# Kernel tuning notes

Measured on AMD Instinct MI355X. Metric: run time of the kernel, lower is better.

Reference implementation:

```python
import jax, jax.numpy as jnp
import numpy as np

N, E, D, R = 50000, 800000, 128, 200


def setup_inputs() -> dict:
    key = jax.random.key(0)
    ks = jax.random.split(key, 8)
    h = jax.random.normal(ks[0], (N, D), jnp.float32)
    emb_rel = jax.random.normal(ks[1], (R, D), jnp.float32)
    loop_weight = jax.random.normal(ks[2], (D, D), jnp.float32) * 0.05
    attn_fc_w = jax.random.normal(ks[3], (D, 3 * D), jnp.float32) * 0.05  # Linear(3D,D) weight [D,3D]
    attn_fc2_w = jax.random.normal(ks[4], (1, D), jnp.float32) * 0.05     # Linear(D,1) weight [1,D]
    src = jax.random.randint(ks[5], (E,), 0, N)
    dst = jax.random.randint(ks[6], (E,), 0, N)
    etype = jax.random.randint(ks[7], (E,), 0, R)
    return {"h": h, "emb_rel": emb_rel, "loop_weight": loop_weight,
            "attn_fc_w": attn_fc_w, "attn_fc2_w": attn_fc2_w,
            "src": src, "dst": dst, "etype": etype}


def reference(h, emb_rel, loop_weight, attn_fc_w, attn_fc2_w, src, dst, etype):
    num_nodes = h.shape[0]
    # attn_fc(concat([h_src, h_dst, rel])) == h_src@Ws.T + h_dst@Wd.T + rel@Wr.T
    # (avoids materializing the [E, 3D] concat)
    Ws, Wd, Wr = jnp.split(attn_fc_w, 3, axis=1)  # each [D, D]
    hs = h[src]  # [E, D] gathered source features
    a = hs @ Ws.T + h[dst] @ Wd.T + emb_rel[etype] @ Wr.T  # [E, D]
    e = jax.nn.leaky_relu((a @ attn_fc2_w.T)[:, 0], 0.01)  # [E] edge logits
    # segment softmax over destination node (stable)
    m = jax.ops.segment_max(e, dst, num_segments=num_nodes)
    w = jnp.exp(e - m[dst])
    denom = jax.ops.segment_sum(w, dst, num_segments=num_nodes)
    alpha = w / denom[dst]  # [E]
    # weighted scatter-sum of source features into destination nodes
    agg = jax.ops.segment_sum(alpha[:, None] * hs, dst, num_segments=num_nodes)
    # DGL update_all leaves zero-in-degree nodes' feature unchanged
    deg = jax.ops.segment_sum(jnp.ones_like(e), dst, num_segments=num_nodes)
    agg = jnp.where(deg[:, None] > 0, agg, h)
    # self-loop message
    return agg + h @ loop_weight
```

## Files before the change

### kernel.cpp

```cpp
#include <hip/hip_runtime.h>

#define D 128
#define TD 384
#define TN 64
#define U  8

__global__ void k_prep(const float* __restrict__ A, const float* __restrict__ v,
                       float* __restrict__ p) {
  __shared__ float vs[D];
  int t = threadIdx.x;
  if (t < D) vs[t] = v[t];
  __syncthreads();
  float acc = 0.f;
#pragma unroll 8
  for (int i = 0; i < D; ++i) acc += vs[i] * A[i * TD + t];
  p[t] = acc;
}

__global__ __launch_bounds__(256) void k_sl(const float* __restrict__ h,
                                            const float* __restrict__ lw,
                                            float* __restrict__ sl, int N) {
  __shared__ float W[D * D];
  int t = threadIdx.x;
  for (int i = t; i < D * D / 4; i += 256)
    ((float4*)W)[i] = ((const float4*)lw)[i];
  __syncthreads();
  int qc = t & 31;
  int slot = t >> 5;
  int ntiles = (N + TN - 1) / TN;
  for (int tile = blockIdx.x; tile < ntiles; tile += gridDim.x) {
    int base = tile * TN + slot * U;
    float4 acc[U];
#pragma unroll
    for (int u = 0; u < U; ++u) acc[u] = make_float4(0.f, 0.f, 0.f, 0.f);
    if ((tile + 1) * TN <= N) {
      for (int k4 = 0; k4 < D / 4; ++k4) {
        int k = k4 * 4;
        float4 w0 = ((const float4*)(W + (size_t)(k + 0) * D))[qc];
        float4 w1 = ((const float4*)(W + (size_t)(k + 1) * D))[qc];
        float4 w2 = ((const float4*)(W + (size_t)(k + 2) * D))[qc];
        float4 w3 = ((const float4*)(W + (size_t)(k + 3) * D))[qc];
#pragma unroll
        for (int u = 0; u < U; ++u) {
          float4 hv = *(const float4*)(h + (size_t)(base + u) * D + k);
          acc[u].x = fmaf(hv.x, w0.x, fmaf(hv.y, w1.x, fmaf(hv.z, w2.x, fmaf(hv.w, w3.x, acc[u].x))));
          acc[u].y = fmaf(hv.x, w0.y, fmaf(hv.y, w1.y, fmaf(hv.z, w2.y, fmaf(hv.w, w3.y, acc[u].y))));
          acc[u].z = fmaf(hv.x, w0.z, fmaf(hv.y, w1.z, fmaf(hv.z, w2.z, fmaf(hv.w, w3.z, acc[u].z))));
          acc[u].w = fmaf(hv.x, w0.w, fmaf(hv.y, w1.w, fmaf(hv.z, w2.w, fmaf(hv.w, w3.w, acc[u].w))));
        }
      }
#pragma unroll
      for (int u = 0; u < U; ++u)
        ((float4*)(sl + (size_t)(base + u) * D))[qc] = acc[u];
    } else {
      for (int k4 = 0; k4 < D / 4; ++k4) {
        int k = k4 * 4;
        float4 w0 = ((const float4*)(W + (size_t)(k + 0) * D))[qc];
        float4 w1 = ((const float4*)(W + (size_t)(k + 1) * D))[qc];
        float4 w2 = ((const float4*)(W + (size_t)(k + 2) * D))[qc];
        float4 w3 = ((const float4*)(W + (size_t)(k + 3) * D))[qc];
#pragma unroll
        for (int u = 0; u < U; ++u) {
          if (base + u < N) {
            float4 hv = *(const float4*)(h + (size_t)(base + u) * D + k);
            acc[u].x = fmaf(hv.x, w0.x, fmaf(hv.y, w1.x, fmaf(hv.z, w2.x, fmaf(hv.w, w3.x, acc[u].x))));
            acc[u].y = fmaf(hv.x, w0.y, fmaf(hv.y, w1.y, fmaf(hv.z, w2.y, fmaf(hv.w, w3.y, acc[u].y))));
            acc[u].z = fmaf(hv.x, w0.z, fmaf(hv.y, w1.z, fmaf(hv.z, w2.z, fmaf(hv.w, w3.z, acc[u].z))));
            acc[u].w = fmaf(hv.x, w0.w, fmaf(hv.y, w1.w, fmaf(hv.z, w2.w, fmaf(hv.w, w3.w, acc[u].w))));
          }
        }
      }
#pragma unroll
      for (int u = 0; u < U; ++u)
        if (base + u < N)
          ((float4*)(sl + (size_t)(base + u) * D))[qc] = acc[u];
    }
  }
}

__global__ void k_scores_hist(const float* __restrict__ h, const float* __restrict__ emb,
                              const float* __restrict__ p, const int* __restrict__ dst,
                              float* __restrict__ ss, float* __restrict__ sd,
                              float* __restrict__ sr, int* __restrict__ cnt,
                              int N, int R, int E, int nbScore) {
  int t = threadIdx.x;
  if ((int)blockIdx.x < nbScore) {
    __shared__ float pl[TD];
    pl[t] = p[t];
    if (t < TD - 256) pl[256 + t] = p[256 + t];
    __syncthreads();
    int w = blockIdx.x * 4 + (t >> 6);
    int l = t & 63;
    if (w < N) {
      float x0 = h[(size_t)w * D + l];
      float x1 = h[(size_t)w * D + 64 + l];
      float a = x0 * pl[l] + x1 * pl[64 + l];
      float b = x0 * pl[128 + l] + x1 * pl[192 + l];
#pragma unroll
      for (int o = 32; o; o >>= 1) { a += __shfl_xor(a, o); b += __shfl_xor(b, o); }
      if (l == 0) { ss[w] = a; sd[w] = b; }
    } else if (w < N + R) {
      int r = w - N;
      float x0 = emb[(size_t)r * D + l];
      float x1 = emb[(size_t)r * D + 64 + l];
      float c = x0 * pl[256 + l] + x1 * pl[320 + l];
#pragma unroll
      for (int o = 32; o; o >>= 1) c += __shfl_xor(c, o);
      if (l == 0) sr[r] = c;
    }
  } else {
    int i = (blockIdx.x - nbScore) * 256 + t;
    int stride = (gridDim.x - nbScore) * 256;
    for (; i < E; i += stride) atomicAdd(&cnt[dst[i]], 1);
  }
}

__global__ void k_scan1(int* __restrict__ cnt, int* __restrict__ bsum, int N) {
  __shared__ int wsum[16];
  int t = threadIdx.x, lane = t & 63, wid = t >> 6;
  int i = blockIdx.x * 1024 + t;
  int v = (i < N) ? cnt[i] : 0;
  int x = v;
#pragma unroll
  for (int o = 1; o < 64; o <<= 1) {
    int y = __shfl_up(x, o);
    if (lane >= o) x += y;
  }
  if (lane == 63) wsum[wid] = x;
  __syncthreads();
  if (t < 16) {
    int y = wsum[t];
#pragma unroll
    for (int o = 1; o < 16; o <<= 1) {
      int z = __shfl_up(y, o);
      if (t >= o) y += z;
    }
    wsum[t] = y;
  }
  __syncthreads();
  int woff = wid ? wsum[wid - 1] : 0;
  if (i < N) cnt[i] = woff + x - v;
  if (t == 0) bsum[blockIdx.x] = wsum[15];
}

__global__ void k_scan2(int* __restrict__ bsum, int nsb) {
  int l = threadIdx.x;
  int v = (l < nsb) ? bsum[l] : 0;
  int x = v;
#pragma unroll
  for (int o = 1; o < 64; o <<= 1) {
    int y = __shfl_up(x, o);
    if (l >= o) x += y;
  }
  if (l < nsb) bsum[l] = x - v;
}

__global__ void k_scan3(const int* __restrict__ bsum, int* __restrict__ cnt,
                        int* __restrict__ cur, int N, int E) {
  int i = blockIdx.x * 1024 + threadIdx.x;
  if (i < N) {
    int v = cnt[i] + bsum[blockIdx.x];
    cnt[i] = v;
    cur[i] = v;
  }
  if (i == 0) cnt[N] = E;
}

__global__ void k_edge(const int* __restrict__ src, const int* __restrict__ dst,
                       const int* __restrict__ et, const float* __restrict__ ss,
                       const float* __restrict__ sd, const float* __restrict__ sr,
                       int* __restrict__ cur, float* __restrict__ esort,
                       int* __restrict__ ssort, int E) {
  int i = blockIdx.x * blockDim.x + threadIdx.x;
  if (i >= E) return;
  int s = src[i], d = dst[i], r = et[i];
  float e = ss[s] + sd[d] + sr[r];
  e = (e > 0.f) ? e : 0.01f * e;
  int pos = atomicAdd(&cur[d], 1);
  esort[pos] = e;
  ssort[pos] = s;
}

__global__ __launch_bounds__(256) void k_agg(const float* __restrict__ h,
                                             const int* __restrict__ off,
                                             const float* __restrict__ esort,
                                             const int* __restrict__ ssort,
                                             const float* __restrict__ sl,
                                             float* __restrict__ out, int N) {
  int n = blockIdx.x;
  int t = threadIdx.x;
  int start = off[n], deg = off[n + 1] - start;
  int qc = t & 31;
  int slot = t >> 5;
  if (deg == 0) {
    if (slot == 0) {
      float4 hv = ((const float4*)(h + (size_t)n * D))[qc];
      float4 sv = ((const float4*)(sl + (size_t)n * D))[qc];
      hv.x += sv.x; hv.y += sv.y; hv.z += sv.z; hv.w += sv.w;
      ((float4*)(out + (size_t)n * D))[qc] = hv;
    }
    return;
  }
  __shared__ float4 part[8][32];
  __shared__ float dpart[8];
  __shared__ float mred[4];

  float m = -3.4e38f;
  for (int i = t; i < deg; i += 256) m = fmaxf(m, esort[start + i]);
#pragma unroll
  for (int o = 32; o; o >>= 1) m = fmaxf(m, __shfl_xor(m, o));
  if ((t & 63) == 0) mred[t >> 6] = m;
  __syncthreads();
  m = fmaxf(fmaxf(mred[0], mred[1]), fmaxf(mred[2], mred[3]));

  float4 acc = {0.f, 0.f, 0.f, 0.f};
  float wpriv = 0.f;
  for (int i = slot; i < deg; i += 8) {
    float w = __expf(esort[start + i] - m);
    int s = ssort[start + i];
    float4 hv = ((const float4*)(h + (size_t)s * D))[qc];
    acc.x = fmaf(w, hv.x, acc.x);
    acc.y = fmaf(w, hv.y, acc.y);
    acc.z = fmaf(w, hv.z, acc.z);
    acc.w = fmaf(w, hv.w, acc.w);
    wpriv += w;
  }
  part[slot][qc] = acc;
  if (qc == 0) dpart[slot] = wpriv;
  __syncthreads();
  if (slot == 0) {
    float4 s4 = part[0][qc];
#pragma unroll
    for (int s2 = 1; s2 < 8; ++s2) {
      float4 p4 = part[s2][qc];
      s4.x += p4.x; s4.y += p4.y; s4.z += p4.z; s4.w += p4.w;
    }
    float denom = ((dpart[0] + dpart[1]) + (dpart[2] + dpart[3])) +
                  ((dpart[4] + dpart[5]) + (dpart[6] + dpart[7]));
    float inv = 1.f / denom;
    float4 sv = ((const float4*)(sl + (size_t)n * D))[qc];
    float4 r;
    r.x = fmaf(s4.x, inv, sv.x);
    r.y = fmaf(s4.y, inv, sv.y);
    r.z = fmaf(s4.z, inv, sv.z);
    r.w = fmaf(s4.w, inv, sv.w);
    ((float4*)(out + (size_t)n * D))[qc] = r;
  }
}

extern "C" void kernel_launch(void* const* d_in, const int* in_sizes, int n_in,
                              void* d_out, int out_size, void* d_ws, size_t ws_size,
                              hipStream_t stream) {
  const float* h   = (const float*)d_in[0];
  const float* emb = (const float*)d_in[1];
  const float* lw  = (const float*)d_in[2];
  const float* afw = (const float*)d_in[3];
  const float* af2 = (const float*)d_in[4];
  const int* src = (const int*)d_in[5];
  const int* dst = (const int*)d_in[6];
  const int* et  = (const int*)d_in[7];
  int N = in_sizes[0] / D;
  int R = in_sizes[1] / D;
  int E = in_sizes[5];
  float* out = (float*)d_out;

  char* ws = (char*)d_ws;
  size_t o = 0;
  auto alloc = [&](size_t bytes) -> void* {
    void* pp = ws + o;
    o = (o + bytes + 255) & ~(size_t)255;
    return pp;
  };
  float* p     = (float*)alloc((size_t)TD * 4);
  float* ss    = (float*)alloc((size_t)N * 4);
  float* sd    = (float*)alloc((size_t)N * 4);
  float* srel  = (float*)alloc((size_t)R * 4);
  int*   cnt   = (int*)  alloc((size_t)(N + 1) * 4);
  int*   cur   = (int*)  alloc((size_t)N * 4);
  int*   bsum  = (int*)  alloc((size_t)64 * 4);
  float* esort = (float*)alloc((size_t)E * 4);
  int*   ssort = (int*)  alloc((size_t)E * 4);
  float* slws  = (float*)alloc((size_t)N * D * 4);

  int nsb = (N + 1023) / 1024;
  int ntiles = (N + TN - 1) / TN;

  hipMemsetAsync(cnt, 0, (size_t)(N + 1) * 4, stream);
  k_prep<<<1, TD, 0, stream>>>(afw, af2, p);
  k_sl<<<ntiles, 256, 0, stream>>>(h, lw, slws, N);
  int nbScore = (N + R + 3) / 4;
  int nbHist = 2048;
  k_scores_hist<<<nbScore + nbHist, 256, 0, stream>>>(h, emb, p, dst, ss, sd, srel,
                                                      cnt, N, R, E, nbScore);
  k_scan1<<<nsb, 1024, 0, stream>>>(cnt, bsum, N);
  k_scan2<<<1, 64, 0, stream>>>(bsum, nsb);
  k_scan3<<<nsb, 1024, 0, stream>>>(bsum, cnt, cur, N, E);
  k_edge<<<(E + 255) / 256, 256, 0, stream>>>(src, dst, et, ss, sd, srel, cur,
                                              esort, ssort, E);
  k_agg<<<N, 256, 0, stream>>>(h, cnt, esort, ssort, slws, out, N);
}
```

Before: 333.5 us.

## Assign one wavefront per node in aggregation and pack edge logit with source

The aggregation kernel now handles four destination nodes per 256-thread block, one 64-lane wavefront each, instead of one node per block. Partial sums are reduced with cross-lane shuffles rather than shared memory and __syncthreads. The edge logit and source index are also packed into one int2 array, so each edge costs a single 8-byte load. This removes block-level sync and the idle threads seen at average degree around 16, but it gives each node only two edge slots in flight, which may reduce memory-level parallelism per node.

```diff
diff --git a/kernel.cpp b/kernel.cpp
--- a/kernel.cpp
+++ b/kernel.cpp
@@ -169,31 +169,33 @@
 __global__ void k_edge(const int* __restrict__ src, const int* __restrict__ dst,
                        const int* __restrict__ et, const float* __restrict__ ss,
                        const float* __restrict__ sd, const float* __restrict__ sr,
-                       int* __restrict__ cur, float* __restrict__ esort,
-                       int* __restrict__ ssort, int E) {
+                       int* __restrict__ cur, int2* __restrict__ epack, int E) {
   int i = blockIdx.x * blockDim.x + threadIdx.x;
   if (i >= E) return;
   int s = src[i], d = dst[i], r = et[i];
   float e = ss[s] + sd[d] + sr[r];
   e = (e > 0.f) ? e : 0.01f * e;
   int pos = atomicAdd(&cur[d], 1);
-  esort[pos] = e;
-  ssort[pos] = s;
-}
-
-__global__ __launch_bounds__(256) void k_agg(const float* __restrict__ h,
-                                             const int* __restrict__ off,
-                                             const float* __restrict__ esort,
-                                             const int* __restrict__ ssort,
-                                             const float* __restrict__ sl,
-                                             float* __restrict__ out, int N) {
-  int n = blockIdx.x;
-  int t = threadIdx.x;
+  int2 pk;
+  pk.x = __float_as_int(e);
+  pk.y = s;
+  epack[pos] = pk;
+}
+
+__global__ __launch_bounds__(256, 8) void k_agg(const float* __restrict__ h,
+                                                const int* __restrict__ off,
+                                                const int2* __restrict__ epack,
+                                                const float* __restrict__ sl,
+                                                float* __restrict__ out, int N) {
+  int n = blockIdx.x * 4 + (threadIdx.x >> 6);
+  if (n >= N) return;
+  int l = threadIdx.x & 63;
+  int qc = l & 31;
+  int es = l >> 5;
   int start = off[n], deg = off[n + 1] - start;
-  int qc = t & 31;
-  int slot = t >> 5;
+
   if (deg == 0) {
-    if (slot == 0) {
+    if (es == 0) {
       float4 hv = ((const float4*)(h + (size_t)n * D))[qc];
       float4 sv = ((const float4*)(sl + (size_t)n * D))[qc];
       hv.x += sv.x; hv.y += sv.y; hv.z += sv.z; hv.w += sv.w;
@@ -201,49 +203,38 @@
     }
     return;
   }
-  __shared__ float4 part[8][32];
-  __shared__ float dpart[8];
-  __shared__ float mred[4];
 
   float m = -3.4e38f;
-  for (int i = t; i < deg; i += 256) m = fmaxf(m, esort[start + i]);
+  for (int i = l; i < deg; i += 64) m = fmaxf(m, __int_as_float(epack[start + i].x));
 #pragma unroll
   for (int o = 32; o; o >>= 1) m = fmaxf(m, __shfl_xor(m, o));
-  if ((t & 63) == 0) mred[t >> 6] = m;
-  __syncthreads();
-  m = fmaxf(fmaxf(mred[0], mred[1]), fmaxf(mred[2], mred[3]));
 
   float4 acc = {0.f, 0.f, 0.f, 0.f};
-  float wpriv = 0.f;
-  for (int i = slot; i < deg; i += 8) {
-    float w = __expf(esort[start + i] - m);
-    int s = ssort[start + i];
-    float4 hv = ((const float4*)(h + (size_t)s * D))[qc];
+  float wsum = 0.f;
+  for (int i = es; i < deg; i += 2) {
+    int2 pk = epack[start + i];
+    float w = __expf(__int_as_float(pk.x) - m);
+    float4 hv = ((const float4*)(h + (size_t)pk.y * D))[qc];
     acc.x = fmaf(w, hv.x, acc.x);
     acc.y = fmaf(w, hv.y, acc.y);
     acc.z = fmaf(w, hv.z, acc.z);
     acc.w = fmaf(w, hv.w, acc.w);
-    wpriv += w;
-  }
-  part[slot][qc] = acc;
-  if (qc == 0) dpart[slot] = wpriv;
-  __syncthreads();
-  if (slot == 0) {
-    float4 s4 = part[0][qc];
-#pragma unroll
-    for (int s2 = 1; s2 < 8; ++s2) {
-      float4 p4 = part[s2][qc];
-      s4.x += p4.x; s4.y += p4.y; s4.z += p4.z; s4.w += p4.w;
-    }
-    float denom = ((dpart[0] + dpart[1]) + (dpart[2] + dpart[3])) +
-                  ((dpart[4] + dpart[5]) + (dpart[6] + dpart[7]));
-    float inv = 1.f / denom;
+    wsum += w;
+  }
+  acc.x += __shfl_xor(acc.x, 32);
+  acc.y += __shfl_xor(acc.y, 32);
+  acc.z += __shfl_xor(acc.z, 32);
+  acc.w += __shfl_xor(acc.w, 32);
+  wsum  += __shfl_xor(wsum, 32);
+
+  if (es == 0) {
+    float inv = 1.f / wsum;
     float4 sv = ((const float4*)(sl + (size_t)n * D))[qc];
     float4 r;
-    r.x = fmaf(s4.x, inv, sv.x);
-    r.y = fmaf(s4.y, inv, sv.y);
-    r.z = fmaf(s4.z, inv, sv.z);
-    r.w = fmaf(s4.w, inv, sv.w);
+    r.x = fmaf(acc.x, inv, sv.x);
+    r.y = fmaf(acc.y, inv, sv.y);
+    r.z = fmaf(acc.z, inv, sv.z);
+    r.w = fmaf(acc.w, inv, sv.w);
     ((float4*)(out + (size_t)n * D))[qc] = r;
   }
 }
@@ -278,8 +269,7 @@
   int*   cnt   = (int*)  alloc((size_t)(N + 1) * 4);
   int*   cur   = (int*)  alloc((size_t)N * 4);
   int*   bsum  = (int*)  alloc((size_t)64 * 4);
-  float* esort = (float*)alloc((size_t)E * 4);
-  int*   ssort = (int*)  alloc((size_t)E * 4);
+  int2*  epack = (int2*) alloc((size_t)E * 8);
   float* slws  = (float*)alloc((size_t)N * D * 4);
 
   int nsb = (N + 1023) / 1024;
@@ -296,6 +286,6 @@
   k_scan2<<<1, 64, 0, stream>>>(bsum, nsb);
   k_scan3<<<nsb, 1024, 0, stream>>>(bsum, cnt, cur, N, E);
   k_edge<<<(E + 255) / 256, 256, 0, stream>>>(src, dst, et, ss, sd, srel, cur,
-                                              esort, ssort, E);
-  k_agg<<<N, 256, 0, stream>>>(h, cnt, esort, ssort, slws, out, N);
-}
+                                              epack, E);
+  k_agg<<<(N + 3) / 4, 256, 0, stream>>>(h, cnt, epack, slws, out, N);
+}
```

Result: faster. 313.2 us (-6.1%).
